# Kernel optimization log

Measured on AMD Instinct MI355X. Metric: run time of the kernel, lower is better.

Reference implementation:

```python
import jax, jax.numpy as jnp
import numpy as np

GROUPS = 32
EPS = 1e-5
HEADS = 8
HEAD_DIM = 40
INNER = HEADS * HEAD_DIM  # 320
QUERY_DIM = 320
CONTEXT_DIM = 768


def setup_inputs() -> dict:
    key = jax.random.key(0)
    ks = jax.random.split(key, 9)
    B, C, H, W = 16, QUERY_DIM, 64, 64
    Lc = 77
    x = jax.random.normal(ks[0], (B, C, H, W), dtype=jnp.float32)
    context = jax.random.normal(ks[1], (B, Lc, CONTEXT_DIM), dtype=jnp.float32)
    # Linear weights in torch layout (out_features, in_features), no bias for q/k/v
    Wq = jax.random.normal(ks[2], (INNER, QUERY_DIM), dtype=jnp.float32) * (QUERY_DIM ** -0.5)
    Wk = jax.random.normal(ks[3], (INNER, CONTEXT_DIM), dtype=jnp.float32) * (CONTEXT_DIM ** -0.5)
    Wv = jax.random.normal(ks[4], (INNER, CONTEXT_DIM), dtype=jnp.float32) * (CONTEXT_DIM ** -0.5)
    Wo = jax.random.normal(ks[5], (QUERY_DIM, INNER), dtype=jnp.float32) * (INNER ** -0.5)
    bo = jnp.zeros((QUERY_DIM,), dtype=jnp.float32)
    gn_scale = jnp.ones((QUERY_DIM,), dtype=jnp.float32)
    gn_bias = jnp.zeros((QUERY_DIM,), dtype=jnp.float32)
    return {"x": x, "context": context, "Wq": Wq, "Wk": Wk, "Wv": Wv,
            "Wo": Wo, "bo": bo, "gn_scale": gn_scale, "gn_bias": gn_bias}


def _group_norm(x, scale, bias):
    # x: [B, C, H, W]
    B, C, H, W = x.shape
    xg = x.reshape(B, GROUPS, C // GROUPS, H, W)
    mean = jnp.mean(xg, axis=(2, 3, 4), keepdims=True)
    var = jnp.var(xg, axis=(2, 3, 4), keepdims=True)
    xn = ((xg - mean) * jax.lax.rsqrt(var + EPS)).reshape(B, C, H, W)
    return xn * scale[None, :, None, None] + bias[None, :, None, None]


def reference(x, context, Wq, Wk, Wv, Wo, bo, gn_scale, gn_bias):
    B, C, H, W = x.shape
    residual = x
    xn = _group_norm(x, gn_scale, gn_bias)
    # (B, C, H, W) -> (B, H*W, C)
    tokens = xn.reshape(B, C, H * W).transpose(0, 2, 1)
    S = H * W
    Lc = context.shape[1]
    scale = HEAD_DIM ** -0.5
    # projections (Linear: x @ W.T); split heads -> [B, h, S, d]
    q = jnp.einsum('bsc,ec->bse', tokens, Wq).reshape(B, S, HEADS, HEAD_DIM).transpose(0, 2, 1, 3)
    k = jnp.einsum('blc,ec->ble', context, Wk).reshape(B, Lc, HEADS, HEAD_DIM).transpose(0, 2, 1, 3)
    v = jnp.einsum('blc,ec->ble', context, Wv).reshape(B, Lc, HEADS, HEAD_DIM).transpose(0, 2, 1, 3)
    scores = jnp.einsum('bhsd,bhkd->bhsk', q, k) * scale  # [B, h, S, Lc]
    attn = jax.nn.softmax(scores, axis=-1)
    out = jnp.einsum('bhsk,bhkd->bhsd', attn, v)  # [B, h, S, d]
    out = out.transpose(0, 2, 1, 3).reshape(B, S, INNER)
    out = jnp.einsum('bse,ce->bsc', out, Wo) + bo  # to_out (dropout is identity at eval)
    out = out.transpose(0, 2, 1).reshape(B, C, H, W)
    return out + residual
```

## Files before the change

### kernel.cpp

```cpp
#include <hip/hip_runtime.h>
#include <hip/hip_bf16.h>
#include <stdint.h>

#define B_    16
#define C_    320
#define S_    4096
#define G_    32
#define LC    77
#define CTX   768
#define HEADS 8
#define HD    40

typedef __bf16 bf16x8_t __attribute__((ext_vector_type(8)));
typedef float  f32x4_t  __attribute__((ext_vector_type(4)));

__device__ __forceinline__ unsigned short f2bf(float f) {
    union { float f; unsigned int u; } v; v.f = f;
    unsigned int r = v.u + 0x7fffu + ((v.u >> 16) & 1u);
    return (unsigned short)(r >> 16);
}
__device__ __forceinline__ float bf2f(unsigned short h) {
    union { unsigned int u; float f; } v; v.u = ((unsigned int)h) << 16;
    return v.f;
}

__device__ __forceinline__ void gload16(const void* g, void* l) {
    __builtin_amdgcn_global_load_lds(
        (const __attribute__((address_space(1))) unsigned int*)g,
        (__attribute__((address_space(3))) unsigned int*)l, 16, 0, 0);
}

__global__ __launch_bounds__(256) void gn_stats(const float* __restrict__ x,
                                                float2* __restrict__ mr) {
    int bg = blockIdx.x;
    const float4* p = (const float4*)(x + (size_t)bg * 40960);
    float s = 0.f, s2 = 0.f;
    for (int i = threadIdx.x; i < 10240; i += 256) {
        float4 v = p[i];
        s  += v.x + v.y + v.z + v.w;
        s2 += v.x * v.x + v.y * v.y + v.z * v.z + v.w * v.w;
    }
    for (int o = 32; o; o >>= 1) {
        s  += __shfl_down(s, o);
        s2 += __shfl_down(s2, o);
    }
    __shared__ float2 red[4];
    int lane = threadIdx.x & 63, wid = threadIdx.x >> 6;
    if (lane == 0) red[wid] = make_float2(s, s2);
    __syncthreads();
    if (threadIdx.x == 0) {
        float a = 0.f, c = 0.f;
        for (int i = 0; i < 4; i++) { a += red[i].x; c += red[i].y; }
        float mean = a / 40960.f;
        float var  = c / 40960.f - mean * mean;
        mr[bg] = make_float2(mean, rsqrtf(var + 1e-5f));
    }
}

__global__ __launch_bounds__(256) void castw(const float* __restrict__ s,
                                             unsigned short* __restrict__ d) {
    int i = blockIdx.x * 256 + threadIdx.x;
    float4 v = ((const float4*)s)[i];
    ushort4 o;
    o.x = f2bf(v.x); o.y = f2bf(v.y); o.z = f2bf(v.z); o.w = f2bf(v.w);
    ((ushort4*)d)[i] = o;
}

__global__ __launch_bounds__(256) void norm_tr(const float* __restrict__ x,
                                               const float2* __restrict__ mr,
                                               const float* __restrict__ gns,
                                               const float* __restrict__ gnb,
                                               unsigned short* __restrict__ tok) {
    int s0 = blockIdx.x * 32, c0 = blockIdx.y * 32, b = blockIdx.z;
    __shared__ unsigned short t[32][33];
    int tx = threadIdx.x & 31, ty = threadIdx.x >> 5;
    #pragma unroll
    for (int i = 0; i < 4; i++) {
        int cl = i * 8 + ty;
        int c = c0 + cl;
        float2 m = mr[b * 32 + c / 10];
        float v = x[((size_t)(b * 320 + c)) * 4096 + s0 + tx];
        v = (v - m.x) * m.y * gns[c] + gnb[c];
        t[cl][tx] = f2bf(v);
    }
    __syncthreads();
    #pragma unroll
    for (int i = 0; i < 4; i++) {
        int sl = i * 8 + ty;
        tok[((size_t)b * 4096 + s0 + sl) * 320 + c0 + tx] = t[tx][sl];
    }
}

__global__ __launch_bounds__(256) void ukern(const float* __restrict__ Wk,
                                             const float* __restrict__ Wq,
                                             unsigned short* __restrict__ Ut) {
    int c = blockIdx.x, h = blockIdx.y;
    int t = threadIdx.x;
    float a0 = 0.f, a1 = 0.f, a2 = 0.f;
    for (int d = 0; d < HD; d++) {
        float wq = Wq[(size_t)(h * HD + d) * 320 + c];
        const float* wkr = Wk + (size_t)(h * HD + d) * CTX;
        a0 += wq * wkr[t];
        a1 += wq * wkr[t + 256];
        a2 += wq * wkr[t + 512];
    }
    unsigned short* o = Ut + ((size_t)h * 320 + c) * CTX;
    o[t]       = f2bf(a0);
    o[t + 256] = f2bf(a1);
    o[t + 512] = f2bf(a2);
}

__global__ __launch_bounds__(256) void kvM_gemm(const float* __restrict__ ctx,
                                                const float* __restrict__ Wv,
                                                const unsigned short* __restrict__ Ut,
                                                unsigned short* __restrict__ vout,
                                                unsigned short* __restrict__ Mout) {
    __shared__ unsigned short la[64][32], lb[64][32];
    int bm = blockIdx.x, bn = blockIdx.y;
    int tid = threadIdx.x, lane = tid & 63, wid = tid >> 6;
    int wm = wid >> 1, wn = wid & 1;
    int lr = tid >> 2, lc = (tid & 3) * 8;
    int fr = lane & 15, kk = (lane >> 4) * 8;

    int arow = bm * 64 + lr; if (arow > 1231) arow = 1231;
    const float* ap = ctx + (size_t)arow * CTX;
    bool isV = (bn < 5);
    const float* wp = isV ? (Wv + (size_t)(bn * 64 + lr) * CTX) : nullptr;
    const unsigned short* up = isV ? nullptr
        : (Ut + ((size_t)((bn - 5) / 5) * 320 + (size_t)((bn - 5) % 5) * 64 + lr) * CTX);

    f32x4_t acc[2][2] = {};
    for (int k0 = 0; k0 < CTX; k0 += 32) {
        float4 a4 = *(const float4*)&ap[k0 + lc];
        float4 a5 = *(const float4*)&ap[k0 + lc + 4];
        ushort4 pa0 = { f2bf(a4.x), f2bf(a4.y), f2bf(a4.z), f2bf(a4.w) };
        ushort4 pa1 = { f2bf(a5.x), f2bf(a5.y), f2bf(a5.z), f2bf(a5.w) };
        *(ushort4*)&la[lr][lc]     = pa0;
        *(ushort4*)&la[lr][lc + 4] = pa1;
        if (isV) {
            float4 w4 = *(const float4*)&wp[k0 + lc];
            float4 w5 = *(const float4*)&wp[k0 + lc + 4];
            ushort4 pw0 = { f2bf(w4.x), f2bf(w4.y), f2bf(w4.z), f2bf(w4.w) };
            ushort4 pw1 = { f2bf(w5.x), f2bf(w5.y), f2bf(w5.z), f2bf(w5.w) };
            *(ushort4*)&lb[lr][lc]     = pw0;
            *(ushort4*)&lb[lr][lc + 4] = pw1;
        } else {
            *(uint4*)&lb[lr][lc] = *(const uint4*)&up[k0 + lc];
        }
        __syncthreads();
        bf16x8_t a0 = *(const bf16x8_t*)&la[wm * 32 + fr][kk];
        bf16x8_t a1 = *(const bf16x8_t*)&la[wm * 32 + 16 + fr][kk];
        bf16x8_t b0 = *(const bf16x8_t*)&lb[wn * 32 + fr][kk];
        bf16x8_t b1 = *(const bf16x8_t*)&lb[wn * 32 + 16 + fr][kk];
        acc[0][0] = __builtin_amdgcn_mfma_f32_16x16x32_bf16(a0, b0, acc[0][0], 0, 0, 0);
        acc[0][1] = __builtin_amdgcn_mfma_f32_16x16x32_bf16(a0, b1, acc[0][1], 0, 0, 0);
        acc[1][0] = __builtin_amdgcn_mfma_f32_16x16x32_bf16(a1, b0, acc[1][0], 0, 0, 0);
        acc[1][1] = __builtin_amdgcn_mfma_f32_16x16x32_bf16(a1, b1, acc[1][1], 0, 0, 0);
        __syncthreads();
    }
    int rg = (lane >> 4) * 4;
    #pragma unroll
    for (int mf = 0; mf < 2; mf++)
        #pragma unroll
        for (int nf = 0; nf < 2; nf++)
            #pragma unroll
            for (int r = 0; r < 4; r++) {
                int row = bm * 64 + wm * 32 + mf * 16 + rg + r;
                if (row < 1232) {
                    int coloff = wn * 32 + nf * 16 + fr;
                    unsigned short val = f2bf(acc[mf][nf][r]);
                    if (isV) {
                        vout[(size_t)row * 320 + bn * 64 + coloff] = val;
                    } else {
                        int bb = row / 77, kv = row - bb * 77;
                        int hh = (bn - 5) / 5;
                        int c = ((bn - 5) % 5) * 64 + coloff;
                        size_t tile = ((size_t)bb * 8 + hh) * 25600;
                        int idx16 = kv * 40 + (c >> 3);
                        int swz = idx16 ^ (kv & 7);
                        Mout[tile + (size_t)swz * 8 + (c & 7)] = val;
                    }
                }
            }
}

__global__ __launch_bounds__(256, 2) void attn4(const unsigned short* __restrict__ tok,
                                                const unsigned short* __restrict__ M,
                                                const unsigned short* __restrict__ v,
                                                unsigned short* __restrict__ att) {
    __shared__ unsigned short Msr[25600];
    __shared__ unsigned short Vt[48][104];
    unsigned short (*Ps)[104] = (unsigned short (*)[104])Msr;

    int tid = threadIdx.x;
    int qt = blockIdx.x, b = blockIdx.y;
    int q0 = qt * 128;
    int lane = tid & 63, wv = tid >> 6;
    int fr = lane & 15, fg = lane >> 4;
    const float scale = 0.15811388300841898f;

    {
        uint4 z = {0, 0, 0, 0};
        uint4* p = (uint4*)&Vt[0][0];
        for (int i = tid; i < 624; i += 256) p[i] = z;
    }

    {
        const unsigned short* Mt = M + ((size_t)b * 8 + 0) * 25600;
        #pragma unroll
        for (int i = 0; i < 13; i++) {
            int u = i * 256 + tid;
            if (u < 3200) gload16(Mt + (size_t)u * 8, &Msr[u * 8]);
        }
    }

    uint4 vreg0, vreg1;
    {
        int r = tid / 5, sg = tid % 5;
        vreg0 = *(const uint4*)&v[((size_t)(b * LC + r)) * 320 + sg * 8];
        int idx = tid + 256;
        if (idx < 385) {
            r = idx / 5; sg = idx % 5;
            vreg1 = *(const uint4*)&v[((size_t)(b * LC + r)) * 320 + sg * 8];
        }
    }

    bf16x8_t atok[2][10];
    const size_t tokbase = ((size_t)b * S_ + q0) * 320;
    #pragma unroll
    for (int mf = 0; mf < 2; mf++)
        #pragma unroll
        for (int k = 0; k < 10; k++)
            atok[mf][k] = *(const bf16x8_t*)&tok[tokbase + (size_t)(wv * 32 + mf * 16 + fr) * 320 + k * 32 + fg * 8];

    __syncthreads();

    for (int h = 0; h < 8; h++) {
        {
            unsigned short e[8];
            int r = tid / 5, sg = tid % 5;
            *(uint4*)e = vreg0;
            #pragma unroll
            for (int j = 0; j < 8; j++) Vt[sg * 8 + j][r] = e[j];
            int idx = tid + 256;
            if (idx < 385) {
                r = idx / 5; sg = idx % 5;
                *(uint4*)e = vreg1;
                #pragma unroll
                for (int j = 0; j < 8; j++) Vt[sg * 8 + j][r] = e[j];
            }
        }
        if (h < 7) {
            int r = tid / 5, sg = tid % 5;
            vreg0 = *(const uint4*)&v[((size_t)(b * LC + r)) * 320 + (h + 1) * HD + sg * 8];
            int idx = tid + 256;
            if (idx < 385) {
                r = idx / 5; sg = idx % 5;
                vreg1 = *(const uint4*)&v[((size_t)(b * LC + r)) * 320 + (h + 1) * HD + sg * 8];
            }
        }

        f32x4_t sc[2][5] = {};
        #pragma unroll
        for (int k = 0; k < 10; k++) {
            bf16x8_t bb[5];
            #pragma unroll
            for (int nf = 0; nf < 5; nf++) {
                int idx16 = (nf * 16 + fr) * 40 + k * 4 + fg;
                bb[nf] = *(const bf16x8_t*)&Msr[(size_t)(idx16 ^ (fr & 7)) * 8];
            }
            #pragma unroll
            for (int mf = 0; mf < 2; mf++)
                #pragma unroll
                for (int nf = 0; nf < 5; nf++)
                    sc[mf][nf] = __builtin_amdgcn_mfma_f32_16x16x32_bf16(atok[mf][k], bb[nf], sc[mf][nf], 0, 0, 0);
        }
        __syncthreads();

        {
            uint4 z = {0, 0, 0, 0};
            int zr = wv * 32 + (lane >> 1);
            *(uint4*)((char*)&Ps[zr][80] + (lane & 1) * 16) = z;
        }

        float mx[2][4], sm[2][4];
        #pragma unroll
        for (int mf = 0; mf < 2; mf++)
            #pragma unroll
            for (int r = 0; r < 4; r++) {
                float m = -1e30f;
                #pragma unroll
                for (int nf = 0; nf < 5; nf++) {
                    float s = sc[mf][nf][r] * scale;
                    if (nf * 16 + fr >= LC) s = -1e30f;
                    sc[mf][nf][r] = s;
                    m = fmaxf(m, s);
                }
                mx[mf][r] = m;
            }
        #pragma unroll
        for (int off = 1; off < 16; off <<= 1)
            #pragma unroll
            for (int mf = 0; mf < 2; mf++)
                #pragma unroll
                for (int r = 0; r < 4; r++)
                    mx[mf][r] = fmaxf(mx[mf][r], __shfl_xor(mx[mf][r], off));
        #pragma unroll
        for (int mf = 0; mf < 2; mf++)
            #pragma unroll
            for (int r = 0; r < 4; r++) {
                float s = 0.f;
                #pragma unroll
                for (int nf = 0; nf < 5; nf++) {
                    float p = __expf(sc[mf][nf][r] - mx[mf][r]);
                    sc[mf][nf][r] = p;
                    s += p;
                }
                sm[mf][r] = s;
            }
        #pragma unroll
        for (int off = 1; off < 16; off <<= 1)
            #pragma unroll
            for (int mf = 0; mf < 2; mf++)
                #pragma unroll
                for (int r = 0; r < 4; r++)
                    sm[mf][r] += __shfl_xor(sm[mf][r], off);

        #pragma unroll
        for (int mf = 0; mf < 2; mf++)
            #pragma unroll
            for (int nf = 0; nf < 5; nf++)
                #pragma unroll
                for (int r = 0; r < 4; r++)
                    Ps[wv * 32 + mf * 16 + fg * 4 + r][nf * 16 + fr] = f2bf(sc[mf][nf][r]);

        f32x4_t ov[2][3] = {};
        #pragma unroll
        for (int ks = 0; ks < 3; ks++) {
            bf16x8_t vb[3];
            #pragma unroll
            for (int nf = 0; nf < 3; nf++)
                vb[nf] = *(const bf16x8_t*)&Vt[nf * 16 + fr][ks * 32 + fg * 8];
            #pragma unroll
            for (int mf = 0; mf < 2; mf++) {
                bf16x8_t pa = *(const bf16x8_t*)&Ps[wv * 32 + mf * 16 + fr][ks * 32 + fg * 8];
                #pragma unroll
                for (int nf = 0; nf < 3; nf++)
                    ov[mf][nf] = __builtin_amdgcn_mfma_f32_16x16x32_bf16(pa, vb[nf], ov[mf][nf], 0, 0, 0);
            }
        }
        __syncthreads();

        if (h < 7) {
            const unsigned short* Mn = M + ((size_t)b * 8 + h + 1) * 25600;
            #pragma unroll
            for (int i = 0; i < 13; i++) {
                int u = i * 256 + tid;
                if (u < 3200) gload16(Mn + (size_t)u * 8, &Msr[u * 8]);
            }
        }

        #pragma unroll
        for (int mf = 0; mf < 2; mf++) {
            float inv[4];
            #pragma unroll
            for (int r = 0; r < 4; r++) inv[r] = 1.f / sm[mf][r];
            #pragma unroll
            for (int nf = 0; nf < 3; nf++) {
                int d = nf * 16 + fr;
                if (d < HD) {
                    #pragma unroll
                    for (int r = 0; r < 4; r++) {
                        int qrow = q0 + wv * 32 + mf * 16 + fg * 4 + r;
                        att[((size_t)(b * S_ + qrow)) * 320 + h * HD + d] = f2bf(ov[mf][nf][r] * inv[r]);
                    }
                }
            }
        }
        __syncthreads();
    }
}

__global__ __launch_bounds__(256) void gemm_oproj2(const unsigned short* __restrict__ att,
                                                   const unsigned short* __restrict__ wo,
                                                   const float* __restrict__ bo,
                                                   const float* __restrict__ resid,
                                                   float* __restrict__ out) {
    __shared__ unsigned short lw[320 * 40];
    __shared__ unsigned short la[64 * 40];
    int tid = threadIdx.x, lane = tid & 63, wv = tid >> 6;
    int fr = lane & 15, fg = lane >> 4;
    int bm = blockIdx.x, b = blockIdx.y;
    int s0 = bm * 64;
    const size_t abase = ((size_t)b * S_ + s0) * 320;

    f32x4_t acc[5][4] = {};

    for (int k0 = 0; k0 < 320; k0 += 32) {
        #pragma unroll
        for (int i = 0; i < 7; i++) {
            int u = i * 256 + tid;
            if (u < 1600) {
                int row = u / 5, ch = u % 5;
                int c = ch < 4 ? ch : 0;
                gload16(wo + (size_t)row * 320 + k0 + c * 8, &lw[(size_t)u * 8]);
            }
        }
        {
            int u = tid;
            int row = u / 5, ch = u % 5;
            int c = ch < 4 ? ch : 0;
            gload16(att + abase + (size_t)row * 320 + k0 + c * 8, &la[(size_t)u * 8]);
            u = tid + 256;
            if (u < 320) {
                row = u / 5; ch = u % 5; c = ch < 4 ? ch : 0;
                gload16(att + abase + (size_t)row * 320 + k0 + c * 8, &la[(size_t)u * 8]);
            }
        }
        __syncthreads();
        bf16x8_t bfrag[4];
        #pragma unroll
        for (int sf = 0; sf < 4; sf++)
            bfrag[sf] = *(const bf16x8_t*)&la[(sf * 16 + fr) * 40 + fg * 8];
        #pragma unroll
        for (int nf = 0; nf < 5; nf++) {
            bf16x8_t afrag = *(const bf16x8_t*)&lw[(wv * 80 + nf * 16 + fr) * 40 + fg * 8];
            #pragma unroll
            for (int sf = 0; sf < 4; sf++)
                acc[nf][sf] = __builtin_amdgcn_mfma_f32_16x16x32_bf16(afrag, bfrag[sf], acc[nf][sf], 0, 0, 0);
        }
        __syncthreads();
    }

    int nbase = wv * 80;
    #pragma unroll
    for (int nf = 0; nf < 5; nf++) {
        #pragma unroll
        for (int r = 0; r < 4; r++) {
            int n = nbase + nf * 16 + fg * 4 + r;
            float bov = bo[n];
            size_t rowb = ((size_t)(b * 320 + n)) * 4096 + s0;
            #pragma unroll
            for (int sf = 0; sf < 4; sf++) {
                int s = sf * 16 + fr;
                out[rowb + s] = acc[nf][sf][r] + bov + resid[rowb + s];
            }
        }
    }
}

extern "C" void kernel_launch(void* const* d_in, const int* in_sizes, int n_in,
                              void* d_out, int out_size, void* d_ws, size_t ws_size,
                              hipStream_t stream) {
    const float* x    = (const float*)d_in[0];
    const float* ctx  = (const float*)d_in[1];
    const float* Wq   = (const float*)d_in[2];
    const float* Wk   = (const float*)d_in[3];
    const float* Wv   = (const float*)d_in[4];
    const float* Wo   = (const float*)d_in[5];
    const float* bo   = (const float*)d_in[6];
    const float* gns  = (const float*)d_in[7];
    const float* gnb  = (const float*)d_in[8];
    float* out = (float*)d_out;

    char* ws = (char*)d_ws;
    float2*         mr    = (float2*)(ws + 0);
    unsigned short* wo_bf = (unsigned short*)(ws + 4096);
    unsigned short* v_bf  = (unsigned short*)(ws + 208896);
    unsigned short* Mbuf  = (unsigned short*)(ws + 997376);
    unsigned short* tok   = (unsigned short*)(ws + 7550976);
    unsigned short* att   = (unsigned short*)(ws + 49494016);
    unsigned short* Ut    = att;

    gn_stats<<<512, 256, 0, stream>>>(x, mr);
    castw<<<100, 256, 0, stream>>>(Wo, wo_bf);
    ukern<<<dim3(320, 8), 256, 0, stream>>>(Wk, Wq, Ut);
    kvM_gemm<<<dim3(20, 45), 256, 0, stream>>>(ctx, Wv, Ut, v_bf, Mbuf);
    norm_tr<<<dim3(128, 10, 16), 256, 0, stream>>>(x, mr, gns, gnb, tok);
    attn4<<<dim3(32, 16), 256, 0, stream>>>(tok, Mbuf, v_bf, att);
    gemm_oproj2<<<dim3(64, 16), 256, 0, stream>>>(att, wo_bf, bo, x, out);
}
```

Measured before the change: 184.1 us.

## Split attention heads across grid z, alias V into LDS, drop max-subtraction

The attention kernel now launches two blocks per (query tile, batch), each handling four heads, so the grid doubles from 512 to 1024 blocks. The V-transpose buffer is aliased into the M shared-memory region, cutting LDS use enough to allow three blocks per CU. The softmax drops the running-max pass and masks padded keys directly, and the per-head output is stored head-major so the output-projection GEMM reads it with new indexing. The cost is that the token tile is loaded twice per batch tile, and skipping max subtraction risks overflow for large scores.

Result: slower. 327.8 us (+78.1%).

```diff
diff --git a/kernel.cpp b/kernel.cpp
--- a/kernel.cpp
+++ b/kernel.cpp
@@ -184,47 +184,39 @@
             }
 }
 
-__global__ __launch_bounds__(256, 2) void attn4(const unsigned short* __restrict__ tok,
+__global__ __launch_bounds__(256, 3) void attn5(const unsigned short* __restrict__ tok,
                                                 const unsigned short* __restrict__ M,
                                                 const unsigned short* __restrict__ v,
                                                 unsigned short* __restrict__ att) {
     __shared__ unsigned short Msr[25600];
-    __shared__ unsigned short Vt[48][104];
     unsigned short (*Ps)[104] = (unsigned short (*)[104])Msr;
+    unsigned short (*Vt)[104] = (unsigned short (*)[104])(Msr + 13312);
 
     int tid = threadIdx.x;
-    int qt = blockIdx.x, b = blockIdx.y;
+    int qt = blockIdx.x, b = blockIdx.y, h0 = blockIdx.z * 4;
     int q0 = qt * 128;
     int lane = tid & 63, wv = tid >> 6;
     int fr = lane & 15, fg = lane >> 4;
     const float scale = 0.15811388300841898f;
 
     {
-        uint4 z = {0, 0, 0, 0};
-        uint4* p = (uint4*)&Vt[0][0];
-        for (int i = tid; i < 624; i += 256) p[i] = z;
-    }
-
-    {
-        const unsigned short* Mt = M + ((size_t)b * 8 + 0) * 25600;
+        const unsigned short* Mt = M + ((size_t)b * 8 + h0) * 25600;
         #pragma unroll
         for (int i = 0; i < 13; i++) {
             int u = i * 256 + tid;
             if (u < 3200) gload16(Mt + (size_t)u * 8, &Msr[u * 8]);
         }
     }
-
     uint4 vreg0, vreg1;
     {
         int r = tid / 5, sg = tid % 5;
-        vreg0 = *(const uint4*)&v[((size_t)(b * LC + r)) * 320 + sg * 8];
+        vreg0 = *(const uint4*)&v[((size_t)(b * LC + r)) * 320 + h0 * HD + sg * 8];
         int idx = tid + 256;
         if (idx < 385) {
             r = idx / 5; sg = idx % 5;
-            vreg1 = *(const uint4*)&v[((size_t)(b * LC + r)) * 320 + sg * 8];
-        }
-    }
-
+            vreg1 = *(const uint4*)&v[((size_t)(b * LC + r)) * 320 + h0 * HD + sg * 8];
+        }
+    }
     bf16x8_t atok[2][10];
     const size_t tokbase = ((size_t)b * S_ + q0) * 320;
     #pragma unroll
@@ -235,7 +227,27 @@
 
     __syncthreads();
 
-    for (int h = 0; h < 8; h++) {
+    #pragma unroll
+    for (int i = 0; i < 4; i++) {
+        int h = h0 + i;
+
+        f32x4_t sc[2][5] = {};
+        #pragma unroll
+        for (int k = 0; k < 10; k++) {
+            bf16x8_t bb[5];
+            #pragma unroll
+            for (int nf = 0; nf < 5; nf++) {
+                int idx16 = (nf * 16 + fr) * 40 + k * 4 + fg;
+                bb[nf] = *(const bf16x8_t*)&Msr[(size_t)(idx16 ^ (fr & 7)) * 8];
+            }
+            #pragma unroll
+            for (int mf = 0; mf < 2; mf++)
+                #pragma unroll
+                for (int nf = 0; nf < 5; nf++)
+                    sc[mf][nf] = __builtin_amdgcn_mfma_f32_16x16x32_bf16(atok[mf][k], bb[nf], sc[mf][nf], 0, 0, 0);
+        }
+        __syncthreads();
+
         {
             unsigned short e[8];
             int r = tid / 5, sg = tid % 5;
@@ -250,7 +262,69 @@
                 for (int j = 0; j < 8; j++) Vt[sg * 8 + j][r] = e[j];
             }
         }
-        if (h < 7) {
+
+        {
+            uint4 z = {0, 0, 0, 0};
+            int zr = wv * 32 + (lane >> 1);
+            *(uint4*)((char*)&Ps[zr][80] + (lane & 1) * 16) = z;
+        }
+
+        float sm[2][4];
+        #pragma unroll
+        for (int mf = 0; mf < 2; mf++)
+            #pragma unroll
+            for (int r = 0; r < 4; r++) {
+                float s = 0.f;
+                #pragma unroll
+                for (int nf = 0; nf < 5; nf++) {
+                    float p = (nf < 4 || fr < 13) ? __expf(sc[mf][nf][r] * scale) : 0.f;
+                    sc[mf][nf][r] = p;
+                    s += p;
+                }
+                sm[mf][r] = s;
+            }
+        #pragma unroll
+        for (int off = 1; off < 16; off <<= 1)
+            #pragma unroll
+            for (int mf = 0; mf < 2; mf++)
+                #pragma unroll
+                for (int r = 0; r < 4; r++)
+                    sm[mf][r] += __shfl_xor(sm[mf][r], off);
+
+        #pragma unroll
+        for (int mf = 0; mf < 2; mf++)
+            #pragma unroll
+            for (int nf = 0; nf < 5; nf++)
+                #pragma unroll
+                for (int r = 0; r < 4; r++)
+                    Ps[wv * 32 + mf * 16 + fg * 4 + r][nf * 16 + fr] = f2bf(sc[mf][nf][r]);
+
+        __syncthreads();
+
+        f32x4_t ov[2][3] = {};
+        #pragma unroll
+        for (int ks = 0; ks < 3; ks++) {
+            bf16x8_t vb[3];
+            #pragma unroll
+            for (int nf = 0; nf < 3; nf++)
+                vb[nf] = *(const bf16x8_t*)&Vt[nf * 16 + fr][ks * 32 + fg * 8];
+            #pragma unroll
+            for (int mf = 0; mf < 2; mf++) {
+                bf16x8_t pa = *(const bf16x8_t*)&Ps[wv * 32 + mf * 16 + fr][ks * 32 + fg * 8];
+                #pragma unroll
+                for (int nf = 0; nf < 3; nf++)
+                    ov[mf][nf] = __builtin_amdgcn_mfma_f32_16x16x32_bf16(pa, vb[nf], ov[mf][nf], 0, 0, 0);
+            }
+        }
+        __syncthreads();
+
+        if (i < 3) {
+            const unsigned short* Mn = M + ((size_t)b * 8 + h + 1) * 25600;
+            #pragma unroll
+            for (int j = 0; j < 13; j++) {
+                int u = j * 256 + tid;
+                if (u < 3200) gload16(Mn + (size_t)u * 8, &Msr[u * 8]);
+            }
             int r = tid / 5, sg = tid % 5;
             vreg0 = *(const uint4*)&v[((size_t)(b * LC + r)) * 320 + (h + 1) * HD + sg * 8];
             int idx = tid + 256;
@@ -260,106 +334,6 @@
             }
         }
 
-        f32x4_t sc[2][5] = {};
-        #pragma unroll
-        for (int k = 0; k < 10; k++) {
-            bf16x8_t bb[5];
-            #pragma unroll
-            for (int nf = 0; nf < 5; nf++) {
-                int idx16 = (nf * 16 + fr) * 40 + k * 4 + fg;
-                bb[nf] = *(const bf16x8_t*)&Msr[(size_t)(idx16 ^ (fr & 7)) * 8];
-            }
-            #pragma unroll
-            for (int mf = 0; mf < 2; mf++)
-                #pragma unroll
-                for (int nf = 0; nf < 5; nf++)
-                    sc[mf][nf] = __builtin_amdgcn_mfma_f32_16x16x32_bf16(atok[mf][k], bb[nf], sc[mf][nf], 0, 0, 0);
-        }
-        __syncthreads();
-
-        {
-            uint4 z = {0, 0, 0, 0};
-            int zr = wv * 32 + (lane >> 1);
-            *(uint4*)((char*)&Ps[zr][80] + (lane & 1) * 16) = z;
-        }
-
-        float mx[2][4], sm[2][4];
-        #pragma unroll
-        for (int mf = 0; mf < 2; mf++)
-            #pragma unroll
-            for (int r = 0; r < 4; r++) {
-                float m = -1e30f;
-                #pragma unroll
-                for (int nf = 0; nf < 5; nf++) {
-                    float s = sc[mf][nf][r] * scale;
-                    if (nf * 16 + fr >= LC) s = -1e30f;
-                    sc[mf][nf][r] = s;
-                    m = fmaxf(m, s);
-                }
-                mx[mf][r] = m;
-            }
-        #pragma unroll
-        for (int off = 1; off < 16; off <<= 1)
-            #pragma unroll
-            for (int mf = 0; mf < 2; mf++)
-                #pragma unroll
-                for (int r = 0; r < 4; r++)
-                    mx[mf][r] = fmaxf(mx[mf][r], __shfl_xor(mx[mf][r], off));
-        #pragma unroll
-        for (int mf = 0; mf < 2; mf++)
-            #pragma unroll
-            for (int r = 0; r < 4; r++) {
-                float s = 0.f;
-                #pragma unroll
-                for (int nf = 0; nf < 5; nf++) {
-                    float p = __expf(sc[mf][nf][r] - mx[mf][r]);
-                    sc[mf][nf][r] = p;
-                    s += p;
-                }
-                sm[mf][r] = s;
-            }
-        #pragma unroll
-        for (int off = 1; off < 16; off <<= 1)
-            #pragma unroll
-            for (int mf = 0; mf < 2; mf++)
-                #pragma unroll
-                for (int r = 0; r < 4; r++)
-                    sm[mf][r] += __shfl_xor(sm[mf][r], off);
-
-        #pragma unroll
-        for (int mf = 0; mf < 2; mf++)
-            #pragma unroll
-            for (int nf = 0; nf < 5; nf++)
-                #pragma unroll
-                for (int r = 0; r < 4; r++)
-                    Ps[wv * 32 + mf * 16 + fg * 4 + r][nf * 16 + fr] = f2bf(sc[mf][nf][r]);
-
-        f32x4_t ov[2][3] = {};
-        #pragma unroll
-        for (int ks = 0; ks < 3; ks++) {
-            bf16x8_t vb[3];
-            #pragma unroll
-            for (int nf = 0; nf < 3; nf++)
-                vb[nf] = *(const bf16x8_t*)&Vt[nf * 16 + fr][ks * 32 + fg * 8];
-            #pragma unroll
-            for (int mf = 0; mf < 2; mf++) {
-                bf16x8_t pa = *(const bf16x8_t*)&Ps[wv * 32 + mf * 16 + fr][ks * 32 + fg * 8];
-                #pragma unroll
-                for (int nf = 0; nf < 3; nf++)
-                    ov[mf][nf] = __builtin_amdgcn_mfma_f32_16x16x32_bf16(pa, vb[nf], ov[mf][nf], 0, 0, 0);
-            }
-        }
-        __syncthreads();
-
-        if (h < 7) {
-            const unsigned short* Mn = M + ((size_t)b * 8 + h + 1) * 25600;
-            #pragma unroll
-            for (int i = 0; i < 13; i++) {
-                int u = i * 256 + tid;
-                if (u < 3200) gload16(Mn + (size_t)u * 8, &Msr[u * 8]);
-            }
-        }
-
         #pragma unroll
         for (int mf = 0; mf < 2; mf++) {
             float inv[4];
@@ -372,12 +346,12 @@
                     #pragma unroll
                     for (int r = 0; r < 4; r++) {
                         int qrow = q0 + wv * 32 + mf * 16 + fg * 4 + r;
-                        att[((size_t)(b * S_ + qrow)) * 320 + h * HD + d] = f2bf(ov[mf][nf][r] * inv[r]);
+                        att[((size_t)(b * 8 + h) * S_ + qrow) * 40 + d] = f2bf(ov[mf][nf][r] * inv[r]);
                     }
                 }
             }
         }
-        __syncthreads();
+        if (i < 3) __syncthreads();
     }
 }
 
@@ -392,7 +366,6 @@
     int fr = lane & 15, fg = lane >> 4;
     int bm = blockIdx.x, b = blockIdx.y;
     int s0 = bm * 64;
-    const size_t abase = ((size_t)b * S_ + s0) * 320;
 
     f32x4_t acc[5][4] = {};
 
@@ -410,11 +383,15 @@
             int u = tid;
             int row = u / 5, ch = u % 5;
             int c = ch < 4 ? ch : 0;
-            gload16(att + abase + (size_t)row * 320 + k0 + c * 8, &la[(size_t)u * 8]);
+            int e0 = k0 + c * 8;
+            gload16(att + ((size_t)(b * 8 + e0 / 40) * S_ + s0 + row) * 40 + e0 % 40,
+                    &la[(size_t)u * 8]);
             u = tid + 256;
             if (u < 320) {
                 row = u / 5; ch = u % 5; c = ch < 4 ? ch : 0;
-                gload16(att + abase + (size_t)row * 320 + k0 + c * 8, &la[(size_t)u * 8]);
+                e0 = k0 + c * 8;
+                gload16(att + ((size_t)(b * 8 + e0 / 40) * S_ + s0 + row) * 40 + e0 % 40,
+                        &la[(size_t)u * 8]);
             }
         }
         __syncthreads();
@@ -477,6 +454,6 @@
     ukern<<<dim3(320, 8), 256, 0, stream>>>(Wk, Wq, Ut);
     kvM_gemm<<<dim3(20, 45), 256, 0, stream>>>(ctx, Wv, Ut, v_bf, Mbuf);
     norm_tr<<<dim3(128, 10, 16), 256, 0, stream>>>(x, mr, gns, gnb, tok);
-    attn4<<<dim3(32, 16), 256, 0, stream>>>(tok, Mbuf, v_bf, att);
+    attn5<<<dim3(32, 16, 2), 256, 0, stream>>>(tok, Mbuf, v_bf, att);
     gemm_oproj2<<<dim3(64, 16), 256, 0, stream>>>(att, wo_bf, bo, x, out);
 }
```
